# Kernel optimization log

Measured on AMD Instinct MI355X. Metric: run time of the kernel, lower is better.

The kernel has to match this reference:

```python
import jax, jax.numpy as jnp
import numpy as np

V, E, R, L = 50257, 256, 1024, 4
B, T = 32, 512
LN_EPS = 1e-5


def setup_inputs() -> dict:
    key = jax.random.key(0)
    ks = jax.random.split(key, 6)
    x = jax.random.randint(ks[0], (B, T), 0, V)
    embed = jax.random.normal(ks[1], (V, E), dtype=jnp.float32)
    # torch init: randn(in, out) / sqrt(in) / 0.9
    Win0 = jax.random.normal(ks[2], (E, R), dtype=jnp.float32) / np.sqrt(E).astype(np.float32) / 0.9
    Win_rest = jax.random.normal(ks[3], (L - 1, R, R), dtype=jnp.float32) / np.sqrt(R).astype(np.float32) / 0.9
    R_stack = jax.random.normal(ks[4], (L, R, R), dtype=jnp.float32) / np.sqrt(R).astype(np.float32) / 0.9
    gamma = jnp.ones((R * L,), dtype=jnp.float32)
    beta = jnp.zeros((R * L,), dtype=jnp.float32)
    return {"x": x, "embed": embed, "Win0": Win0, "Win_rest": Win_rest,
            "R_stack": R_stack, "gamma": gamma, "beta": beta}


def _layer_norm(h, gamma, beta):
    mu = jnp.mean(h, axis=-1, keepdims=True)
    var = jnp.mean(jnp.square(h - mu), axis=-1, keepdims=True)
    return (h - mu) * jax.lax.rsqrt(var + LN_EPS) * gamma + beta


def reference(x, embed, Win0, Win_rest, R_stack, gamma, beta):
    # x: [B,T] int ids. deep_type='deep_esn': layer i>0 takes the *current-step*
    # state of layer i-1 as input; readout concatenates all layer states.
    xe = embed[x]                      # [B,T,E]
    xe = jnp.transpose(xe, (1, 0, 2))  # [T,B,E] for scan over time
    b = x.shape[0]
    n_layers = R_stack.shape[0]
    r = R_stack.shape[1]
    init = tuple(jnp.zeros((b, r), dtype=xe.dtype) for _ in range(n_layers))

    def step(states, emb_t):
        new_states = []
        inp = emb_t
        for i in range(n_layers):
            W = Win0 if i == 0 else Win_rest[i - 1]
            s = jnp.tanh(states[i] @ R_stack[i] + inp @ W)  # [B,R]
            new_states.append(s)
            inp = s  # deep stacking: feed updated state to next layer
        return tuple(new_states), None

    final_states, _ = jax.lax.scan(step, init, xe)
    h = jnp.concatenate(final_states, axis=-1)  # [B, R*L]
    return _layer_norm(h, gamma, beta)
```

## Files before the change

### kernel.cpp

```cpp
#include <hip/hip_runtime.h>
#include <math.h>


#define TT    512
#define RDIM  1024
#define EDIM  256
#define NL    4
#define BB    32
#define NBLK  256
#define JW    16
#define HDIM  (RDIM * NL)
#define NPAN  4
#define CSTRIDE 32

#define S_ELEMS   (2 * NL * NPAN * RDIM * 8)
#define FIN_ELEMS (BB * HDIM)

typedef float vf2 __attribute__((ext_vector_type(2)));
typedef float vf4 __attribute__((ext_vector_type(4)));

__device__ __forceinline__ float dpp_xor1(float x) {
    return __int_as_float(__builtin_amdgcn_mov_dpp(__float_as_int(x), 0xB1, 0xF, 0xF, true));
}
__device__ __forceinline__ float dpp_xor2(float x) {
    return __int_as_float(__builtin_amdgcn_mov_dpp(__float_as_int(x), 0x4E, 0xF, 0xF, true));
}

__device__ __forceinline__ void gload_sc(vf4& d, const void* p) {
    asm volatile("global_load_dwordx4 %0, %1, off sc0 sc1" : "=v"(d) : "v"(p));
}
__device__ __forceinline__ void gload_pl(vf4& d, const void* p) {
    asm volatile("global_load_dwordx4 %0, %1, off" : "=v"(d) : "v"(p));
}
__device__ __forceinline__ void vwait(int wn, vf4& r) {
    if (wn >= 7)      asm volatile("s_waitcnt vmcnt(7)" : "+v"(r));
    else if (wn == 6) asm volatile("s_waitcnt vmcnt(6)" : "+v"(r));
    else if (wn == 5) asm volatile("s_waitcnt vmcnt(5)" : "+v"(r));
    else if (wn == 4) asm volatile("s_waitcnt vmcnt(4)" : "+v"(r));
    else if (wn == 3) asm volatile("s_waitcnt vmcnt(3)" : "+v"(r));
    else if (wn == 2) asm volatile("s_waitcnt vmcnt(2)" : "+v"(r));
    else if (wn == 1) asm volatile("s_waitcnt vmcnt(1)" : "+v"(r));
    else              asm volatile("s_waitcnt vmcnt(0)" : "+v"(r));
}

__global__ void gather_kernel(const int* __restrict__ x,
                              const float* __restrict__ embed,
                              float* __restrict__ xe)
{
    __shared__ int   ids[BB];
    __shared__ float sh[BB * (EDIM + 1)];
    const int t = blockIdx.x, tid = threadIdx.x;
    if (tid < BB) ids[tid] = x[tid * TT + t];
    __syncthreads();
    for (int r = 0; r < BB; ++r)
        sh[r * (EDIM + 1) + tid] = embed[ids[r] * EDIM + tid];
    __syncthreads();
    for (int i = tid; i < NPAN * EDIM * 8; i += 256) {
        int p = i >> 11, k = (i >> 3) & (EDIM - 1), bo = i & 7;
        xe[(size_t)t * (NPAN * EDIM * 8) + i] = sh[(p * 8 + bo) * (EDIM + 1) + k];
    }
}

template<int KIN, bool SCIN>
__device__ __forceinline__ void tick_body(
    const float* __restrict__ Sown, const float* __restrict__ Sin,
    const float* __restrict__ Wlds,
    const int kh, const int lam, const int kq, const int bh,
    vf2 acc[4][8])
{
    constexpr int NOWN = RDIM / 64;
    constexpr int NIN  = KIN / 64;
    constexpr int NT   = NOWN + NIN;

    const vf4* ownp = (const vf4*)Sown;
    const vf4* inp  = (const vf4*)Sin;

    vf4 b[8];

    #pragma unroll
    for (int i = 0; i < 8; ++i)
        gload_sc(b[i], (const void*)(ownp + (size_t)(kh * NOWN + i) * 64 + lam));

    #pragma unroll
    for (int i = 0; i < NT; ++i) {
        vf4& br = b[i & 7];
        const int wn = (NT - 1 - i) < 7 ? (NT - 1 - i) : 7;
        vwait(wn, br);
        const vf4 v = br;
        if (i + 8 < NT) {
            const int n = i + 8;
            if (n < NOWN) {
                gload_sc(br, (const void*)(ownp + (size_t)(kh * NOWN + n) * 64 + lam));
            } else {
                const void* p = (const void*)(inp + (size_t)(kh * NIN + (n - NOWN)) * 64 + lam);
                if (SCIN) gload_sc(br, p);
                else      gload_pl(br, p);
            }
        }
        const int k = (i < NOWN) ? ((kh * NOWN + i) * 32 + kq)
                                 : (RDIM + (kh * NIN + (i - NOWN)) * 32 + kq);
        const float* wr = &Wlds[k * JW + bh * 8];
        float4 wo0 = *(const float4*)wr;
        float4 wo1 = *(const float4*)(wr + 4);
        vf2 wv[8];
        wv[0] = (vf2){wo0.x, wo0.y}; wv[1] = (vf2){wo0.z, wo0.w};
        wv[2] = (vf2){wo1.x, wo1.y}; wv[3] = (vf2){wo1.z, wo1.w};
        wv[4] = (vf2){dpp_xor1(wo0.x), dpp_xor1(wo0.y)};
        wv[5] = (vf2){dpp_xor1(wo0.z), dpp_xor1(wo0.w)};
        wv[6] = (vf2){dpp_xor1(wo1.x), dpp_xor1(wo1.y)};
        wv[7] = (vf2){dpp_xor1(wo1.z), dpp_xor1(wo1.w)};
        const float vv[4] = {v[0], v[1], v[2], v[3]};
        #pragma unroll
        for (int q = 0; q < 4; ++q) {
            vf2 s = {vv[q], vv[q]};
            #pragma unroll
            for (int jp = 0; jp < 8; ++jp) acc[q][jp] += s * wv[jp];
        }
    }
}

__global__ __launch_bounds__(512, 2) void reservoir_kernel(
    const float* __restrict__ Win0, const float* __restrict__ WinR,
    const float* __restrict__ Rst,  const float* __restrict__ xe,
    float* __restrict__ S, float* __restrict__ Fin,
    unsigned* __restrict__ cnt, unsigned* __restrict__ rel)
{
    __shared__ float Wlds[2048 * JW];
    __shared__ float Pbuf[NPAN * JW * 8];
    const int tid   = threadIdx.x;
    const int blk   = blockIdx.x;
    const int layer = blk >> 6;
    const int j0    = (blk & 63) * JW;
    const int Kin   = (layer == 0) ? EDIM : RDIM;

    for (int idx = tid; idx < (RDIM + Kin) * JW; idx += 512) {
        int k = idx >> 4, j = idx & 15;
        float wv;
        if (k < RDIM) wv = Rst[((size_t)layer * RDIM + k) * RDIM + j0 + j];
        else {
            int k2 = k - RDIM;
            wv = (layer == 0) ? Win0[(size_t)k2 * RDIM + j0 + j]
                              : WinR[((size_t)(layer - 1) * RDIM + k2) * RDIM + j0 + j];
        }
        Wlds[idx] = wv;
    }
    __syncthreads();

    const int w8  = tid >> 6;
    const int w   = w8 & 3;
    const int kh  = w8 >> 2;
    const int lam = tid & 63;
    const int kq  = lam >> 1;
    const int bh  = lam & 1;
    const int bh4 = bh * 4;

    for (int tick = 0; tick < TT + NL - 1; ++tick) {
        const int t = tick - layer;
        if (t >= 0 && t < TT) {
            const int cur = tick & 1, prv = (tick - 1) & 1;
            const float* Sown = S + (((size_t)(prv * NL + layer)) * NPAN + w) * RDIM * 8;
            const float* Sin  = (layer == 0)
                ? (xe + ((size_t)t * NPAN + w) * (EDIM * 8))
                : (S + (((size_t)(prv * NL + layer - 1)) * NPAN + w) * RDIM * 8);

            vf2 acc[4][8];
            #pragma unroll
            for (int i = 0; i < 4; ++i)
                #pragma unroll
                for (int jp = 0; jp < 8; ++jp) acc[i][jp] = (vf2)(0.f);

            if (layer == 0) tick_body<EDIM, false>(Sown, Sin, Wlds, kh, lam, kq, bh, acc);
            else            tick_body<RDIM, true >(Sown, Sin, Wlds, kh, lam, kq, bh, acc);

            float r64v[64];
            #pragma unroll
            for (int i = 0; i < 4; ++i)
                #pragma unroll
                for (int jp = 0; jp < 8; ++jp) {
                    r64v[(i << 4) | (jp << 1)]     = acc[i][jp].x;
                    r64v[(i << 4) | (jp << 1) | 1] = acc[i][jp].y;
                }
            float r32v[32], r16v[16], r8v[8], r4v[4], rfin[2];
            {   const bool myb = kq & 1;
                #pragma unroll
                for (int m = 0; m < 32; ++m) {
                    float a = r64v[2 * m], b = r64v[2 * m + 1];
                    float send = myb ? a : b, keep = myb ? b : a;
                    r32v[m] = keep + dpp_xor2(send);
                }
            }
            {   const bool myb = (kq >> 1) & 1;
                #pragma unroll
                for (int m = 0; m < 16; ++m) {
                    float a = r32v[2 * m], b = r32v[2 * m + 1];
                    float send = myb ? a : b, keep = myb ? b : a;
                    r16v[m] = keep + __shfl_xor(send, 4, 64);
                }
            }
            {   const bool myb = (kq >> 2) & 1;
                #pragma unroll
                for (int m = 0; m < 8; ++m) {
                    float a = r16v[2 * m], b = r16v[2 * m + 1];
                    float send = myb ? a : b, keep = myb ? b : a;
                    r8v[m] = keep + __shfl_xor(send, 8, 64);
                }
            }
            {   const bool myb = (kq >> 3) & 1;
                #pragma unroll
                for (int m = 0; m < 4; ++m) {
                    float a = r8v[2 * m], b = r8v[2 * m + 1];
                    float send = myb ? a : b, keep = myb ? b : a;
                    r4v[m] = keep + __shfl_xor(send, 16, 64);
                }
            }
            {   const bool myb = (kq >> 4) & 1;
                #pragma unroll
                for (int m = 0; m < 2; ++m) {
                    float a = r4v[2 * m], b = r4v[2 * m + 1];
                    float send = myb ? a : b, keep = myb ? b : a;
                    rfin[m] = keep + __shfl_xor(send, 32, 64);
                }
            }

            const int i0 = kq >> 4;
            const int cc = kq & 15;
            const int j  = (cc & 7) + 8 * (bh ^ (cc >> 3));
            if (kh) {
                #pragma unroll
                for (int m = 0; m < 2; ++m)
                    Pbuf[(w * JW + j) * 8 + (bh4 + i0 + 2 * m)] = rfin[m];
            }
            __syncthreads();
            if (!kh) {
                float* sbase = S + (((size_t)(cur * NL + layer)) * NPAN + w) * RDIM * 8
                                 + (size_t)(j0 + j) * 8;
                #pragma unroll
                for (int m = 0; m < 2; ++m) {
                    const int bi = bh4 + i0 + 2 * m;
                    const float o = tanhf(rfin[m] + Pbuf[(w * JW + j) * 8 + bi]);
                    __hip_atomic_store(sbase + bi, o, __ATOMIC_RELAXED, __HIP_MEMORY_SCOPE_AGENT);
                    if (t == TT - 1)
                        Fin[(size_t)(w * 8 + bi) * HDIM + layer * RDIM + j0 + j] = o;
                }
            }
        }
        __syncthreads();
        if (tid == 0)
            __hip_atomic_fetch_add(&cnt[(blk & 15) * CSTRIDE], 1u,
                                   __ATOMIC_RELAXED, __HIP_MEMORY_SCOPE_AGENT);
        const unsigned wrel = (unsigned)(tick + 1);
        if (blk == 0) {
            if (tid < 64) {
                const unsigned wsum = wrel * (unsigned)NBLK;
                int guard = 0;
                for (;;) {
                    unsigned v = 0;
                    if (lam < 16)
                        v = __hip_atomic_load(&cnt[lam * CSTRIDE],
                                              __ATOMIC_RELAXED, __HIP_MEMORY_SCOPE_AGENT);
                    #pragma unroll
                    for (int m = 1; m <= 32; m <<= 1) v += __shfl_xor(v, m, 64);
                    if (v >= wsum) break;
                    __builtin_amdgcn_s_sleep(2);
                    if (++guard > (1 << 16)) break;
                }
                if (lam < 16)
                    __hip_atomic_store(&rel[lam * CSTRIDE], wrel,
                                       __ATOMIC_RELAXED, __HIP_MEMORY_SCOPE_AGENT);
            }
        } else {
            if (tid == 0) {
                int guard = 0;
                while (__hip_atomic_load(&rel[(blk & 15) * CSTRIDE],
                                         __ATOMIC_RELAXED, __HIP_MEMORY_SCOPE_AGENT) < wrel) {
                    __builtin_amdgcn_s_sleep(4);
                    if (++guard > (1 << 16)) break;
                }
            }
        }
        __syncthreads();
    }
}

__global__ void ln_kernel(const float* __restrict__ Fin,
                          const float* __restrict__ gamma,
                          const float* __restrict__ beta,
                          float* __restrict__ out)
{
    const int r = blockIdx.x, tid = threadIdx.x;
    const float* row = Fin + (size_t)r * HDIM;
    float s = 0.f, s2 = 0.f;
    for (int i = tid; i < HDIM; i += 256) { float v = row[i]; s += v; s2 += v * v; }
    for (int off = 32; off; off >>= 1) {
        s  += __shfl_down(s,  off, 64);
        s2 += __shfl_down(s2, off, 64);
    }
    __shared__ float rs[4], rs2[4];
    __shared__ float mu_s, rstd_s;
    if ((tid & 63) == 0) { rs[tid >> 6] = s; rs2[tid >> 6] = s2; }
    __syncthreads();
    if (tid == 0) {
        float S1 = rs[0] + rs[1] + rs[2] + rs[3];
        float S2 = rs2[0] + rs2[1] + rs2[2] + rs2[3];
        float mu = S1 / (float)HDIM;
        float var = S2 / (float)HDIM - mu * mu;
        mu_s = mu; rstd_s = rsqrtf(var + 1e-5f);
    }
    __syncthreads();
    float mu = mu_s, rstd = rstd_s;
    for (int i = tid; i < HDIM; i += 256)
        out[(size_t)r * HDIM + i] = (row[i] - mu) * rstd * gamma[i] + beta[i];
}

extern "C" void kernel_launch(void* const* d_in, const int* in_sizes, int n_in,
                              void* d_out, int out_size, void* d_ws, size_t ws_size,
                              hipStream_t stream)
{
    const int*   x     = (const int*)d_in[0];
    const float* embed = (const float*)d_in[1];
    const float* Win0  = (const float*)d_in[2];
    const float* WinR  = (const float*)d_in[3];
    const float* Rst   = (const float*)d_in[4];
    const float* gamma = (const float*)d_in[5];
    const float* beta  = (const float*)d_in[6];
    float* out = (float*)d_out;

    char* ws = (char*)d_ws;
    unsigned* cnt = (unsigned*)ws;
    unsigned* rel = cnt + 16 * CSTRIDE;
    float* S   = (float*)(ws + 8192);
    float* Fin = S + S_ELEMS;
    float* xe  = Fin + FIN_ELEMS;

    hipMemsetAsync(ws, 0, 8192 + (size_t)S_ELEMS * 4, stream);
    gather_kernel   <<<TT,   256, 0, stream>>>(x, embed, xe);
    reservoir_kernel<<<NBLK, 512, 0, stream>>>(Win0, WinR, Rst, xe, S, Fin, cnt, rel);
    ln_kernel       <<<BB,   256, 0, stream>>>(Fin, gamma, beta, out);
}
```

Before: 4.840 ms.

## Split each column group's K reduction across two blocks with global partial exchange

Doubles the persistent grid from 256 to 512 blocks by splitting each layer's 16-column group along K into two halves, so each block holds half the weights in LDS and streams half the state per tick. The kh=1 block writes its partial sums to a global buffer and raises a per-group flag; the kh=0 block spins on that flag, adds the partial, applies tanh and publishes the state. This is meant to cut per-tick latency on the serial recurrence by using more CUs, at the cost of an extra intra-tick global handoff and a wider grid barrier.

```diff
diff --git a/kernel.cpp b/kernel.cpp
--- a/kernel.cpp
+++ b/kernel.cpp
@@ -7,13 +7,14 @@
 #define EDIM  256
 #define NL    4
 #define BB    32
-#define NBLK  256
+#define NBLK  512
 #define JW    16
 #define HDIM  (RDIM * NL)
 #define NPAN  4
 #define CSTRIDE 32
 
 #define S_ELEMS   (2 * NL * NPAN * RDIM * 8)
+#define PG_ELEMS  (NL * 64 * JW * BB)
 #define FIN_ELEMS (BB * HDIM)
 
 typedef float vf2 __attribute__((ext_vector_type(2)));
@@ -61,25 +62,26 @@
     }
 }
 
-template<int KIN, bool SCIN>
+template<int NI, bool SCIN>
 __device__ __forceinline__ void tick_body(
     const float* __restrict__ Sown, const float* __restrict__ Sin,
     const float* __restrict__ Wlds,
-    const int kh, const int lam, const int kq, const int bh,
+    const int ks, const int lam, const int kq, const int bh,
     vf2 acc[4][8])
 {
-    constexpr int NOWN = RDIM / 64;
-    constexpr int NIN  = KIN / 64;
-    constexpr int NT   = NOWN + NIN;
+    constexpr int NOWN = 8;
+    constexpr int NT   = NOWN + NI;
 
     const vf4* ownp = (const vf4*)Sown;
     const vf4* inp  = (const vf4*)Sin;
+    const int wobase = ks * 256;
+    const int wibase = 512 + ks * NI * 32;
 
     vf4 b[8];
 
     #pragma unroll
     for (int i = 0; i < 8; ++i)
-        gload_sc(b[i], (const void*)(ownp + (size_t)(kh * NOWN + i) * 64 + lam));
+        gload_sc(b[i], (const void*)(ownp + (size_t)i * 64 + lam));
 
     #pragma unroll
     for (int i = 0; i < NT; ++i) {
@@ -88,18 +90,13 @@
         vwait(wn, br);
         const vf4 v = br;
         if (i + 8 < NT) {
-            const int n = i + 8;
-            if (n < NOWN) {
-                gload_sc(br, (const void*)(ownp + (size_t)(kh * NOWN + n) * 64 + lam));
-            } else {
-                const void* p = (const void*)(inp + (size_t)(kh * NIN + (n - NOWN)) * 64 + lam);
-                if (SCIN) gload_sc(br, p);
-                else      gload_pl(br, p);
-            }
-        }
-        const int k = (i < NOWN) ? ((kh * NOWN + i) * 32 + kq)
-                                 : (RDIM + (kh * NIN + (i - NOWN)) * 32 + kq);
-        const float* wr = &Wlds[k * JW + bh * 8];
+            const void* p = (const void*)(inp + (size_t)i * 64 + lam);
+            if (SCIN) gload_sc(br, p);
+            else      gload_pl(br, p);
+        }
+        const int wrow = (i < NOWN) ? (wobase + i * 32 + kq)
+                                    : (wibase + (i - NOWN) * 32 + kq);
+        const float* wr = &Wlds[wrow * JW + bh * 8];
         float4 wo0 = *(const float4*)wr;
         float4 wo1 = *(const float4*)(wr + 4);
         vf2 wv[8];
@@ -119,26 +116,85 @@
     }
 }
 
-__global__ __launch_bounds__(512, 2) void reservoir_kernel(
+__device__ __forceinline__ void reduce64(const vf2 acc[4][8], const int kq,
+                                         float rfin[2])
+{
+    float r64v[64];
+    #pragma unroll
+    for (int i = 0; i < 4; ++i)
+        #pragma unroll
+        for (int jp = 0; jp < 8; ++jp) {
+            r64v[(i << 4) | (jp << 1)]     = acc[i][jp].x;
+            r64v[(i << 4) | (jp << 1) | 1] = acc[i][jp].y;
+        }
+    float r32v[32], r16v[16], r8v[8], r4v[4];
+    {   const bool myb = kq & 1;
+        #pragma unroll
+        for (int m = 0; m < 32; ++m) {
+            float a = r64v[2 * m], b = r64v[2 * m + 1];
+            float send = myb ? a : b, keep = myb ? b : a;
+            r32v[m] = keep + dpp_xor2(send);
+        }
+    }
+    {   const bool myb = (kq >> 1) & 1;
+        #pragma unroll
+        for (int m = 0; m < 16; ++m) {
+            float a = r32v[2 * m], b = r32v[2 * m + 1];
+            float send = myb ? a : b, keep = myb ? b : a;
+            r16v[m] = keep + __shfl_xor(send, 4, 64);
+        }
+    }
+    {   const bool myb = (kq >> 2) & 1;
+        #pragma unroll
+        for (int m = 0; m < 8; ++m) {
+            float a = r16v[2 * m], b = r16v[2 * m + 1];
+            float send = myb ? a : b, keep = myb ? b : a;
+            r8v[m] = keep + __shfl_xor(send, 8, 64);
+        }
+    }
+    {   const bool myb = (kq >> 3) & 1;
+        #pragma unroll
+        for (int m = 0; m < 4; ++m) {
+            float a = r8v[2 * m], b = r8v[2 * m + 1];
+            float send = myb ? a : b, keep = myb ? b : a;
+            r4v[m] = keep + __shfl_xor(send, 16, 64);
+        }
+    }
+    {   const bool myb = (kq >> 4) & 1;
+        #pragma unroll
+        for (int m = 0; m < 2; ++m) {
+            float a = r4v[2 * m], b = r4v[2 * m + 1];
+            float send = myb ? a : b, keep = myb ? b : a;
+            rfin[m] = keep + __shfl_xor(send, 32, 64);
+        }
+    }
+}
+
+__global__ __launch_bounds__(512, 4) void reservoir_kernel(
     const float* __restrict__ Win0, const float* __restrict__ WinR,
     const float* __restrict__ Rst,  const float* __restrict__ xe,
-    float* __restrict__ S, float* __restrict__ Fin,
-    unsigned* __restrict__ cnt, unsigned* __restrict__ rel)
-{
-    __shared__ float Wlds[2048 * JW];
+    float* __restrict__ S, float* __restrict__ Pglob, float* __restrict__ Fin,
+    unsigned* __restrict__ cnt, unsigned* __restrict__ rel,
+    unsigned* __restrict__ flagP)
+{
+    __shared__ float Wlds[1024 * JW];
     __shared__ float Pbuf[NPAN * JW * 8];
     const int tid   = threadIdx.x;
     const int blk   = blockIdx.x;
-    const int layer = blk >> 6;
-    const int j0    = (blk & 63) * JW;
+    const int layer = blk >> 7;
+    const int r     = blk & 127;
+    const int g     = r >> 1;
+    const int kh    = r & 1;
+    const int j0    = g * JW;
     const int Kin   = (layer == 0) ? EDIM : RDIM;
-
-    for (int idx = tid; idx < (RDIM + Kin) * JW; idx += 512) {
+    const int KinH  = Kin >> 1;
+
+    for (int idx = tid; idx < (512 + KinH) * JW; idx += 512) {
         int k = idx >> 4, j = idx & 15;
         float wv;
-        if (k < RDIM) wv = Rst[((size_t)layer * RDIM + k) * RDIM + j0 + j];
+        if (k < 512) wv = Rst[((size_t)layer * RDIM + kh * 512 + k) * RDIM + j0 + j];
         else {
-            int k2 = k - RDIM;
+            int k2 = kh * KinH + (k - 512);
             wv = (layer == 0) ? Win0[(size_t)k2 * RDIM + j0 + j]
                               : WinR[((size_t)(layer - 1) * RDIM + k2) * RDIM + j0 + j];
         }
@@ -148,20 +204,24 @@
 
     const int w8  = tid >> 6;
     const int w   = w8 & 3;
-    const int kh  = w8 >> 2;
+    const int ks  = w8 >> 2;
     const int lam = tid & 63;
     const int kq  = lam >> 1;
     const int bh  = lam & 1;
     const int bh4 = bh * 4;
+    const int pgi = layer * 64 + g;
+    float* const pg = Pglob + (size_t)pgi * (JW * BB);
 
     for (int tick = 0; tick < TT + NL - 1; ++tick) {
         const int t = tick - layer;
         if (t >= 0 && t < TT) {
             const int cur = tick & 1, prv = (tick - 1) & 1;
-            const float* Sown = S + (((size_t)(prv * NL + layer)) * NPAN + w) * RDIM * 8;
+            const float* Sown = S + (((size_t)(prv * NL + layer)) * NPAN + w) * RDIM * 8
+                                  + (size_t)(kh * 512 + ks * 256) * 8;
             const float* Sin  = (layer == 0)
-                ? (xe + ((size_t)t * NPAN + w) * (EDIM * 8))
-                : (S + (((size_t)(prv * NL + layer - 1)) * NPAN + w) * RDIM * 8);
+                ? (xe + ((size_t)t * NPAN + w) * (EDIM * 8) + (size_t)(kh * 128 + ks * 64) * 8)
+                : (S + (((size_t)(prv * NL + layer - 1)) * NPAN + w) * RDIM * 8
+                     + (size_t)(kh * 512 + ks * 256) * 8);
 
             vf2 acc[4][8];
             #pragma unroll
@@ -169,78 +229,65 @@
                 #pragma unroll
                 for (int jp = 0; jp < 8; ++jp) acc[i][jp] = (vf2)(0.f);
 
-            if (layer == 0) tick_body<EDIM, false>(Sown, Sin, Wlds, kh, lam, kq, bh, acc);
-            else            tick_body<RDIM, true >(Sown, Sin, Wlds, kh, lam, kq, bh, acc);
-
-            float r64v[64];
-            #pragma unroll
-            for (int i = 0; i < 4; ++i)
-                #pragma unroll
-                for (int jp = 0; jp < 8; ++jp) {
-                    r64v[(i << 4) | (jp << 1)]     = acc[i][jp].x;
-                    r64v[(i << 4) | (jp << 1) | 1] = acc[i][jp].y;
-                }
-            float r32v[32], r16v[16], r8v[8], r4v[4], rfin[2];
-            {   const bool myb = kq & 1;
-                #pragma unroll
-                for (int m = 0; m < 32; ++m) {
-                    float a = r64v[2 * m], b = r64v[2 * m + 1];
-                    float send = myb ? a : b, keep = myb ? b : a;
-                    r32v[m] = keep + dpp_xor2(send);
-                }
-            }
-            {   const bool myb = (kq >> 1) & 1;
-                #pragma unroll
-                for (int m = 0; m < 16; ++m) {
-                    float a = r32v[2 * m], b = r32v[2 * m + 1];
-                    float send = myb ? a : b, keep = myb ? b : a;
-                    r16v[m] = keep + __shfl_xor(send, 4, 64);
-                }
-            }
-            {   const bool myb = (kq >> 2) & 1;
-                #pragma unroll
-                for (int m = 0; m < 8; ++m) {
-                    float a = r16v[2 * m], b = r16v[2 * m + 1];
-                    float send = myb ? a : b, keep = myb ? b : a;
-                    r8v[m] = keep + __shfl_xor(send, 8, 64);
-                }
-            }
-            {   const bool myb = (kq >> 3) & 1;
-                #pragma unroll
-                for (int m = 0; m < 4; ++m) {
-                    float a = r8v[2 * m], b = r8v[2 * m + 1];
-                    float send = myb ? a : b, keep = myb ? b : a;
-                    r4v[m] = keep + __shfl_xor(send, 16, 64);
-                }
-            }
-            {   const bool myb = (kq >> 4) & 1;
-                #pragma unroll
-                for (int m = 0; m < 2; ++m) {
-                    float a = r4v[2 * m], b = r4v[2 * m + 1];
-                    float send = myb ? a : b, keep = myb ? b : a;
-                    rfin[m] = keep + __shfl_xor(send, 32, 64);
-                }
-            }
+            if (layer == 0) tick_body<2, false>(Sown, Sin, Wlds, ks, lam, kq, bh, acc);
+            else            tick_body<8, true >(Sown, Sin, Wlds, ks, lam, kq, bh, acc);
+
+            float rfin[2];
+            reduce64(acc, kq, rfin);
 
             const int i0 = kq >> 4;
             const int cc = kq & 15;
             const int j  = (cc & 7) + 8 * (bh ^ (cc >> 3));
-            if (kh) {
+            if (ks) {
                 #pragma unroll
                 for (int m = 0; m < 2; ++m)
                     Pbuf[(w * JW + j) * 8 + (bh4 + i0 + 2 * m)] = rfin[m];
             }
             __syncthreads();
-            if (!kh) {
-                float* sbase = S + (((size_t)(cur * NL + layer)) * NPAN + w) * RDIM * 8
-                                 + (size_t)(j0 + j) * 8;
+            float p[2];
+            if (!ks) {
                 #pragma unroll
-                for (int m = 0; m < 2; ++m) {
-                    const int bi = bh4 + i0 + 2 * m;
-                    const float o = tanhf(rfin[m] + Pbuf[(w * JW + j) * 8 + bi]);
-                    __hip_atomic_store(sbase + bi, o, __ATOMIC_RELAXED, __HIP_MEMORY_SCOPE_AGENT);
-                    if (t == TT - 1)
-                        Fin[(size_t)(w * 8 + bi) * HDIM + layer * RDIM + j0 + j] = o;
+                for (int m = 0; m < 2; ++m)
+                    p[m] = rfin[m] + Pbuf[(w * JW + j) * 8 + (bh4 + i0 + 2 * m)];
+            }
+
+            if (kh == 1) {
+                if (!ks) {
+                    #pragma unroll
+                    for (int m = 0; m < 2; ++m)
+                        __hip_atomic_store(&pg[(size_t)j * BB + w * 8 + (bh4 + i0 + 2 * m)],
+                                           p[m], __ATOMIC_RELAXED, __HIP_MEMORY_SCOPE_AGENT);
+                }
+                __syncthreads();
+                if (tid == 0)
+                    __hip_atomic_store(&flagP[pgi * CSTRIDE], (unsigned)(tick + 1),
+                                       __ATOMIC_RELAXED, __HIP_MEMORY_SCOPE_AGENT);
+            } else {
+                if (tid == 0) {
+                    int guard = 0;
+                    while (__hip_atomic_load(&flagP[pgi * CSTRIDE],
+                                             __ATOMIC_RELAXED, __HIP_MEMORY_SCOPE_AGENT)
+                           < (unsigned)(tick + 1)) {
+                        __builtin_amdgcn_s_sleep(2);
+                        if (++guard > (1 << 18)) break;
+                    }
+                }
+                __syncthreads();
+                if (!ks) {
+                    float* sbase = S + (((size_t)(cur * NL + layer)) * NPAN + w) * RDIM * 8
+                                     + (size_t)(j0 + j) * 8;
+                    #pragma unroll
+                    for (int m = 0; m < 2; ++m) {
+                        const int bi = bh4 + i0 + 2 * m;
+                        const float q = __uint_as_float(__hip_atomic_load(
+                            (const unsigned*)&pg[(size_t)j * BB + w * 8 + bi],
+                            __ATOMIC_RELAXED, __HIP_MEMORY_SCOPE_AGENT));
+                        const float o = tanhf(p[m] + q);
+                        __hip_atomic_store(sbase + bi, o, __ATOMIC_RELAXED,
+                                           __HIP_MEMORY_SCOPE_AGENT);
+                        if (t == TT - 1)
+                            Fin[(size_t)(w * 8 + bi) * HDIM + layer * RDIM + j0 + j] = o;
+                    }
                 }
             }
         }
@@ -262,7 +309,7 @@
                     for (int m = 1; m <= 32; m <<= 1) v += __shfl_xor(v, m, 64);
                     if (v >= wsum) break;
                     __builtin_amdgcn_s_sleep(2);
-                    if (++guard > (1 << 16)) break;
+                    if (++guard > (1 << 17)) break;
                 }
                 if (lam < 16)
                     __hip_atomic_store(&rel[lam * CSTRIDE], wrel,
@@ -274,7 +321,7 @@
                 while (__hip_atomic_load(&rel[(blk & 15) * CSTRIDE],
                                          __ATOMIC_RELAXED, __HIP_MEMORY_SCOPE_AGENT) < wrel) {
                     __builtin_amdgcn_s_sleep(4);
-                    if (++guard > (1 << 16)) break;
+                    if (++guard > (1 << 17)) break;
                 }
             }
         }
@@ -326,14 +373,17 @@
     float* out = (float*)d_out;
 
     char* ws = (char*)d_ws;
-    unsigned* cnt = (unsigned*)ws;
-    unsigned* rel = cnt + 16 * CSTRIDE;
-    float* S   = (float*)(ws + 8192);
-    float* Fin = S + S_ELEMS;
-    float* xe  = Fin + FIN_ELEMS;
-
-    hipMemsetAsync(ws, 0, 8192 + (size_t)S_ELEMS * 4, stream);
+    unsigned* cnt   = (unsigned*)ws;
+    unsigned* rel   = (unsigned*)(ws + 2048);
+    unsigned* flagP = (unsigned*)(ws + 4096);
+    float* S     = (float*)(ws + 40960);
+    float* Pglob = S + S_ELEMS;
+    float* Fin   = Pglob + PG_ELEMS;
+    float* xe    = Fin + FIN_ELEMS;
+
+    hipMemsetAsync(ws, 0, 40960 + (size_t)S_ELEMS * 4, stream);
     gather_kernel   <<<TT,   256, 0, stream>>>(x, embed, xe);
-    reservoir_kernel<<<NBLK, 512, 0, stream>>>(Win0, WinR, Rst, xe, S, Fin, cnt, rel);
+    reservoir_kernel<<<NBLK, 512, 0, stream>>>(Win0, WinR, Rst, xe, S, Pglob, Fin,
+                                               cnt, rel, flagP);
     ln_kernel       <<<BB,   256, 0, stream>>>(Fin, gamma, beta, out);
 }
```

Measured after the change: 7.801 ms. +61.2%, slower.
